# Optimization experiments

Hardware: AMD Instinct MI355X
Metric: run time of the kernel (lower is better)

Reference implementation:

```python
import jax, jax.numpy as jnp
import numpy as np

N_NODES = 100_000
N_EDGES = 1_250_000
IN_FEATS, N_HIDDEN, N_CLASSES = 64, 64, 32


def setup_inputs() -> dict:
    key = jax.random.key(0)
    ks = jax.random.split(key, 8)
    x = jax.random.normal(ks[0], (N_NODES, IN_FEATS), dtype=jnp.float32)
    src = jax.random.randint(ks[1], (N_EDGES,), 0, N_NODES, dtype=jnp.int64)
    dst = jax.random.randint(ks[2], (N_EDGES,), 0, N_NODES, dtype=jnp.int64)
    s1 = 1.0 / np.sqrt(IN_FEATS)
    s2 = 1.0 / np.sqrt(N_HIDDEN)
    W_self1 = jax.random.normal(ks[3], (IN_FEATS, N_HIDDEN), dtype=jnp.float32) * s1
    W_neigh1 = jax.random.normal(ks[4], (IN_FEATS, N_HIDDEN), dtype=jnp.float32) * s1
    b1 = jnp.zeros((N_HIDDEN,), dtype=jnp.float32)
    W_self2 = jax.random.normal(ks[5], (N_HIDDEN, N_CLASSES), dtype=jnp.float32) * s2
    W_neigh2 = jax.random.normal(ks[6], (N_HIDDEN, N_CLASSES), dtype=jnp.float32) * s2
    b2 = jnp.zeros((N_CLASSES,), dtype=jnp.float32)
    return dict(x=x, src=src, dst=dst, W_self1=W_self1, W_neigh1=W_neigh1, b1=b1,
                W_self2=W_self2, W_neigh2=W_neigh2, b2=b2)


def _sage_conv(h, src, dst, W_self, W_neigh, b):
    # mean aggregation over in-neighbors: gather src feats, segment-sum by dst
    n = h.shape[0]
    msg = h[src]  # [E, d] -- dominant memory traffic
    agg = jax.ops.segment_sum(msg, dst, num_segments=n)
    deg = jax.ops.segment_sum(jnp.ones_like(dst, dtype=h.dtype), dst, num_segments=n)
    h_neigh = agg / jnp.maximum(deg, 1.0)[:, None]  # zero-degree nodes get 0 (DGL behavior)
    return h @ W_self + h_neigh @ W_neigh + b


def reference(x, src, dst, W_self1, W_neigh1, b1, W_self2, W_neigh2, b2):
    h = _sage_conv(x, src, dst, W_self1, W_neigh1, b1)
    h = jax.nn.relu(h)
    # dropout(p=0.5) is identity in eval mode
    return _sage_conv(h, src, dst, W_self2, W_neigh2, b2)
```

## Files before the change

### kernel.cpp

```cpp
#include <hip/hip_runtime.h>
#include <hip/hip_bf16.h>


#define NF 64
#define BW 256
#define BSH 8
#define MAXB 512
#define CAPMAX 8192
#define P1_CHUNK 2048
#define H1S 68

typedef __attribute__((ext_vector_type(8))) short short8;
typedef __attribute__((ext_vector_type(8))) unsigned short ushort8v;
typedef __attribute__((ext_vector_type(4))) float floatx4;

__device__ __forceinline__ short bf16hi(float v) {
    __hip_bfloat16 h = __float2bfloat16(v);
    return *(short*)&h;
}
__device__ __forceinline__ float bf2f(short s) {
    __hip_bfloat16 h = *(__hip_bfloat16*)&s;
    return __bfloat162float(h);
}
__device__ __forceinline__ float bits2f(unsigned short u) {
    unsigned int x = ((unsigned int)u) << 16;
    union { unsigned int i; float f; } c; c.i = x; return c.f;
}


__global__ __launch_bounds__(256) void prep_kernel(
        int* __restrict__ gcursor,
        const float* __restrict__ Ws1, const float* __restrict__ Wn1,
        const float* __restrict__ Ws2, const float* __restrict__ Wn2,
        unsigned short* __restrict__ w1p, unsigned short* __restrict__ w2p) {
    const int tid = threadIdx.x;
    if (blockIdx.x == 0) {
        for (int i = tid; i < MAXB; i += 256) gcursor[i] = 0;
        return;
    }
    const int part = blockIdx.x - 1;
    for (int i = tid; i < 32 * 64; i += 256) {
        int n = part * 32 + (i >> 6), k = i & 63;
        float v = (n < 64) ? Ws1[k * 64 + n] : Wn1[k * 64 + (n - 64)];
        short hv = bf16hi(v);
        w1p[n * 64 + k] = (unsigned short)hv;
        w1p[8192 + n * 64 + k] = (unsigned short)bf16hi(v - bf2f(hv));
    }
    for (int i = tid; i < 16 * 64; i += 256) {
        int n = part * 16 + (i >> 6), k = i & 63;
        float v = (n < 32) ? Ws2[k * 32 + n] : Wn2[k * 32 + (n - 32)];
        short hv = bf16hi(v);
        w2p[n * 64 + k] = (unsigned short)hv;
        w2p[4096 + n * 64 + k] = (unsigned short)bf16hi(v - bf2f(hv));
    }
}


__global__ __launch_bounds__(256) void p1_dense1_kernel(
        const int* __restrict__ src, const int* __restrict__ dst,
        int* __restrict__ gcursor, unsigned* __restrict__ bucket,
        int E, int nbuckets, int dblocks,
        const float* __restrict__ X,
        const unsigned short* __restrict__ w1p,
        const float* __restrict__ bias,
        float* __restrict__ outA,
        unsigned short* __restrict__ outB,
        int N) {
    __shared__ int smem_i[2 * MAXB];
    const int tid = threadIdx.x;

    if ((int)blockIdx.x >= dblocks) {
        int* cnt   = smem_i;
        int* cbase = smem_i + MAXB;
        const int bid = blockIdx.x - dblocks;
        const int beg = bid * P1_CHUNK;
        const int end = min(E, beg + P1_CHUNK);
        for (int i = tid; i < nbuckets; i += 256) cnt[i] = 0;
        __syncthreads();
        for (int e = beg + tid; e < end; e += 256)
            atomicAdd(&cnt[dst[e] >> BSH], 1);
        __syncthreads();
        for (int i = tid; i < nbuckets; i += 256) {
            int c = cnt[i];
            cbase[i] = c ? atomicAdd(&gcursor[i], c) : 0;
            cnt[i] = 0;
        }
        __syncthreads();
        for (int e = beg + tid; e < end; e += 256) {
            int d = dst[e];
            int r = d >> BSH;
            int p = cbase[r] + atomicAdd(&cnt[r], 1);
            if (p < CAPMAX)
                bucket[(size_t)r * CAPMAX + p] = ((unsigned)src[e] << BSH) | (unsigned)(d & (BW - 1));
        }
        return;
    }

    constexpr int NT = 8, NSELF = 4;
    const int lane = tid & 63;
    const int wid  = tid >> 6;
    const int m = lane & 15, quad = lane >> 4;
    const int rowblk = blockIdx.x * 128 + wid * 32;

    floatx4 acc[2][NT];
    #pragma unroll
    for (int rt = 0; rt < 2; ++rt)
        #pragma unroll
        for (int t = 0; t < NT; ++t) acc[rt][t] = (floatx4)(0.f);

    short8 ah[2][2], al[2][2];
    #pragma unroll
    for (int rt = 0; rt < 2; ++rt) {
        int r = rowblk + rt * 16 + m;
        if (r >= N) r = N - 1;
        const float* xp = X + (size_t)r * 64 + quad * 8;
        #pragma unroll
        for (int h = 0; h < 2; ++h) {
            floatx4 f0 = *(const floatx4*)(xp + h * 32);
            floatx4 f1 = *(const floatx4*)(xp + h * 32 + 4);
            short8 hi, lo;
            #pragma unroll
            for (int j = 0; j < 4; ++j) {
                short hv = bf16hi(f0[j]);
                hi[j] = hv; lo[j] = bf16hi(f0[j] - bf2f(hv));
                short hv2 = bf16hi(f1[j]);
                hi[4 + j] = hv2; lo[4 + j] = bf16hi(f1[j] - bf2f(hv2));
            }
            ah[rt][h] = hi; al[rt][h] = lo;
        }
    }

    #pragma unroll
    for (int t = 0; t < NT; ++t) {
        int n = t * 16 + m;
        const unsigned short* ph = w1p + n * 64 + quad * 8;
        const unsigned short* pl = ph + 8192;
        #pragma unroll
        for (int h = 0; h < 2; ++h) {
            short8 bh = *(const short8*)(ph + h * 32);
            short8 bl = *(const short8*)(pl + h * 32);
            #pragma unroll
            for (int rt = 0; rt < 2; ++rt) {
                acc[rt][t] = __builtin_amdgcn_mfma_f32_16x16x32_bf16(ah[rt][h], bh, acc[rt][t], 0, 0, 0);
                acc[rt][t] = __builtin_amdgcn_mfma_f32_16x16x32_bf16(al[rt][h], bh, acc[rt][t], 0, 0, 0);
                acc[rt][t] = __builtin_amdgcn_mfma_f32_16x16x32_bf16(ah[rt][h], bl, acc[rt][t], 0, 0, 0);
            }
        }
    }

    #pragma unroll
    for (int rt = 0; rt < 2; ++rt) {
        #pragma unroll
        for (int t = 0; t < NT; ++t) {
            #pragma unroll
            for (int r4 = 0; r4 < 4; ++r4) {
                int row = rowblk + rt * 16 + quad * 4 + r4;
                if (row < N) {
                    if (t < NSELF) {
                        int col = t * 16 + m;
                        outA[(size_t)row * 64 + col] = acc[rt][t][r4] + bias[col];
                    } else {
                        int col = (t - NSELF) * 16 + m;
                        outB[(size_t)row * 64 + col] = (unsigned short)bf16hi(acc[rt][t][r4]);
                    }
                }
            }
        }
    }
}


__global__ __launch_bounds__(256) void p2_csr_kernel(const unsigned* __restrict__ bucket,
                                                     const int* __restrict__ gcursor,
                                                     int* __restrict__ row_start,
                                                     int* __restrict__ csr_src,
                                                     int N, int nbuckets) {
    __shared__ unsigned stage[CAPMAX];
    __shared__ int cnt[BW];
    __shared__ int excl[BW];
    const int r = blockIdx.x;
    const int tid = threadIdx.x;

    int partial = 0;
    for (int i = tid; i < r; i += 256) partial += min(gcursor[i], CAPMAX);
    excl[tid] = partial;
    __syncthreads();
    for (int off = 128; off > 0; off >>= 1) {
        if (tid < off) excl[tid] += excl[tid + off];
        __syncthreads();
    }
    const int base = excl[0];
    const int sz = min(gcursor[r], CAPMAX);
    const unsigned* bsrc = bucket + (size_t)r * CAPMAX;
    __syncthreads();

    cnt[tid] = 0;
    __syncthreads();
    for (int i = tid; i < sz; i += 256) {
        unsigned v = bsrc[i];
        stage[i] = v;
        atomicAdd(&cnt[v & (BW - 1)], 1);
    }
    __syncthreads();
    excl[tid] = cnt[tid];
    __syncthreads();
    for (int off = 1; off < BW; off <<= 1) {
        int v0 = (tid >= off) ? excl[tid - off] : 0;
        __syncthreads();
        excl[tid] += v0;
        __syncthreads();
    }
    int node = r * BW + tid;
    if (node < N) row_start[node] = base + excl[tid] - cnt[tid];
    if (r == nbuckets - 1 && tid == 0) row_start[N] = base + sz;
    __syncthreads();
    cnt[tid] = excl[tid] - cnt[tid];
    __syncthreads();
    for (int i = tid; i < sz; i += 256) {
        unsigned v = stage[i];
        int p = atomicAdd(&cnt[v & (BW - 1)], 1);
        csr_src[base + p] = (int)(v >> BSH);
    }
}


__global__ __launch_bounds__(256) void agg64_d2_kernel(
        const unsigned short* __restrict__ t1n,
        const float* __restrict__ xs,
        const int* __restrict__ row_start,
        const int* __restrict__ csr_src,
        const unsigned short* __restrict__ w2p,
        const float* __restrict__ b2,
        float* __restrict__ outD,
        unsigned short* __restrict__ t2n,
        int N, int E) {
    __shared__ float h1s[16][H1S];
    const int tid = threadIdx.x;
    const int lane = tid & 63;
    const int wid  = tid >> 6;
    const int half = lane >> 5;
    const int g = (lane >> 3) & 3;
    const int c = lane & 7;
    const int nbase = blockIdx.x * 16;

    const int ln0 = wid * 4 + half;
    const int ln1 = ln0 + 2;
    const int n0 = nbase + ln0, n1 = nbase + ln1;
    int beg0 = 0, end0 = 0, beg1 = 0, end1 = 0;
    if (n0 < N) { beg0 = row_start[n0]; end0 = row_start[n0 + 1]; }
    if (n1 < N) { beg1 = row_start[n1]; end1 = row_start[n1 + 1]; }

    float a0[8] = {0.f, 0.f, 0.f, 0.f, 0.f, 0.f, 0.f, 0.f};
    float a1[8] = {0.f, 0.f, 0.f, 0.f, 0.f, 0.f, 0.f, 0.f};
    int j0 = beg0 + g, j1 = beg1 + g;
    const int Em1 = E - 1;
    int i0 = csr_src[min(j0, Em1)];
    int i1 = csr_src[min(j0 + 4, Em1)];
    int i2 = csr_src[min(j1, Em1)];
    int i3 = csr_src[min(j1 + 4, Em1)];
    while ((j0 < end0) || (j1 < end1)) {
        int s0 = ((unsigned)i0 < (unsigned)N) ? i0 : 0;
        int s1 = ((unsigned)i1 < (unsigned)N) ? i1 : 0;
        int s2 = ((unsigned)i2 < (unsigned)N) ? i2 : 0;
        int s3 = ((unsigned)i3 < (unsigned)N) ? i3 : 0;
        ushort8v u0 = *(const ushort8v*)(t1n + (size_t)s0 * 64 + c * 8);
        ushort8v u1 = *(const ushort8v*)(t1n + (size_t)s1 * 64 + c * 8);
        ushort8v u2 = *(const ushort8v*)(t1n + (size_t)s2 * 64 + c * 8);
        ushort8v u3 = *(const ushort8v*)(t1n + (size_t)s3 * 64 + c * 8);
        i0 = csr_src[min(j0 + 8, Em1)];
        i1 = csr_src[min(j0 + 12, Em1)];
        i2 = csr_src[min(j1 + 8, Em1)];
        i3 = csr_src[min(j1 + 12, Em1)];
        const bool c00 = j0 < end0, c01 = j0 + 4 < end0;
        const bool c10 = j1 < end1, c11 = j1 + 4 < end1;
        #pragma unroll
        for (int i = 0; i < 8; ++i) {
            a0[i] += (c00 ? bits2f(u0[i]) : 0.f) + (c01 ? bits2f(u1[i]) : 0.f);
            a1[i] += (c10 ? bits2f(u2[i]) : 0.f) + (c11 ? bits2f(u3[i]) : 0.f);
        }
        j0 += 8; j1 += 8;
    }

    const int m = lane & 15, quad = lane >> 4;
    const int coln = wid * 16 + m;
    const unsigned short* pb = w2p + coln * 64 + quad * 8;
    short8 bhf0 = *(const short8*)(pb);
    short8 bhf1 = *(const short8*)(pb + 32);
    short8 blf0 = *(const short8*)(pb + 4096);
    short8 blf1 = *(const short8*)(pb + 4096 + 32);

    floatx4 x00 = (floatx4)(0.f), x01 = (floatx4)(0.f);
    floatx4 x10 = (floatx4)(0.f), x11 = (floatx4)(0.f);
    if (g == 0) {
        if (n0 < N) {
            const float* p = xs + (size_t)n0 * 64 + c * 8;
            x00 = *(const floatx4*)p; x01 = *(const floatx4*)(p + 4);
        }
        if (n1 < N) {
            const float* p = xs + (size_t)n1 * 64 + c * 8;
            x10 = *(const floatx4*)p; x11 = *(const floatx4*)(p + 4);
        }
    }

    #pragma unroll
    for (int i = 0; i < 8; ++i) {
        float v = a0[i];
        v += __shfl_xor(v, 8);
        v += __shfl_xor(v, 16);
        a0[i] = v;
        float w = a1[i];
        w += __shfl_xor(w, 8);
        w += __shfl_xor(w, 16);
        a1[i] = w;
    }
    if (g == 0) {
        floatx4 h0, h1v;
        if (n0 < N) {
            float invd = 1.0f / fmaxf((float)(end0 - beg0), 1.0f);
            #pragma unroll
            for (int i = 0; i < 4; ++i) {
                h0[i]  = fmaxf(x00[i] + a0[i] * invd, 0.f);
                h1v[i] = fmaxf(x01[i] + a0[4 + i] * invd, 0.f);
            }
        } else { h0 = (floatx4)(0.f); h1v = (floatx4)(0.f); }
        *(floatx4*)&h1s[ln0][c * 8]     = h0;
        *(floatx4*)&h1s[ln0][c * 8 + 4] = h1v;
        if (n1 < N) {
            float invd = 1.0f / fmaxf((float)(end1 - beg1), 1.0f);
            #pragma unroll
            for (int i = 0; i < 4; ++i) {
                h0[i]  = fmaxf(x10[i] + a1[i] * invd, 0.f);
                h1v[i] = fmaxf(x11[i] + a1[4 + i] * invd, 0.f);
            }
        } else { h0 = (floatx4)(0.f); h1v = (floatx4)(0.f); }
        *(floatx4*)&h1s[ln1][c * 8]     = h0;
        *(floatx4*)&h1s[ln1][c * 8 + 4] = h1v;
    }
    __syncthreads();

    short8 ah[2], al[2];
    #pragma unroll
    for (int h = 0; h < 2; ++h) {
        const float* hp = &h1s[m][quad * 8 + h * 32];
        floatx4 f0 = *(const floatx4*)hp;
        floatx4 f1 = *(const floatx4*)(hp + 4);
        short8 hi, lo;
        #pragma unroll
        for (int j = 0; j < 4; ++j) {
            short hv = bf16hi(f0[j]);
            hi[j] = hv; lo[j] = bf16hi(f0[j] - bf2f(hv));
            short hv2 = bf16hi(f1[j]);
            hi[4 + j] = hv2; lo[4 + j] = bf16hi(f1[j] - bf2f(hv2));
        }
        ah[h] = hi; al[h] = lo;
    }
    floatx4 acc2 = (floatx4)(0.f);
    acc2 = __builtin_amdgcn_mfma_f32_16x16x32_bf16(ah[0], bhf0, acc2, 0, 0, 0);
    acc2 = __builtin_amdgcn_mfma_f32_16x16x32_bf16(al[0], bhf0, acc2, 0, 0, 0);
    acc2 = __builtin_amdgcn_mfma_f32_16x16x32_bf16(ah[0], blf0, acc2, 0, 0, 0);
    acc2 = __builtin_amdgcn_mfma_f32_16x16x32_bf16(ah[1], bhf1, acc2, 0, 0, 0);
    acc2 = __builtin_amdgcn_mfma_f32_16x16x32_bf16(al[1], bhf1, acc2, 0, 0, 0);
    acc2 = __builtin_amdgcn_mfma_f32_16x16x32_bf16(ah[1], blf1, acc2, 0, 0, 0);
    #pragma unroll
    for (int r4 = 0; r4 < 4; ++r4) {
        int node = nbase + quad * 4 + r4;
        if (node < N) {
            if (coln < 32) outD[(size_t)node * 32 + coln] = acc2[r4] + b2[coln];
            else t2n[(size_t)node * 32 + (coln - 32)] = (unsigned short)bf16hi(acc2[r4]);
        }
    }
}


__global__ __launch_bounds__(256) void agg32_kernel(float* io,
                                                    const unsigned short* __restrict__ t2n,
                                                    const int* __restrict__ row_start,
                                                    const int* __restrict__ csr_src,
                                                    int N, int E) {
    const int tid = threadIdx.x;
    const int lane = tid & 63;
    const int wid = tid >> 6;
    const int slot = lane >> 4;
    const int g = (lane >> 2) & 3;
    const int c = lane & 3;
    const int n = blockIdx.x * 16 + wid * 4 + slot;

    int beg = 0, end = 0;
    if (n < N) { beg = row_start[n]; end = row_start[n + 1]; }

    floatx4 s0v = (floatx4)(0.f), s1v = (floatx4)(0.f);
    size_t o = (size_t)n * 32 + c * 8;
    if (n < N && g == 0) {
        s0v = *(const floatx4*)(io + o);
        s1v = *(const floatx4*)(io + o + 4);
    }

    float acc[8] = {0.f, 0.f, 0.f, 0.f, 0.f, 0.f, 0.f, 0.f};
    const int Em1 = E - 1;
    for (int j = beg + g; j < end; j += 8) {
        int j2 = j + 4;
        int s0 = csr_src[j];
        int s1 = csr_src[min(j2, Em1)];
        s0 = ((unsigned)s0 < (unsigned)N) ? s0 : 0;
        s1 = ((unsigned)s1 < (unsigned)N) ? s1 : 0;
        ushort8v u0 = *(const ushort8v*)(t2n + (size_t)s0 * 32 + c * 8);
        ushort8v u1 = *(const ushort8v*)(t2n + (size_t)s1 * 32 + c * 8);
        const bool c1 = j2 < end;
        #pragma unroll
        for (int i = 0; i < 8; ++i)
            acc[i] += bits2f(u0[i]) + (c1 ? bits2f(u1[i]) : 0.f);
    }
    #pragma unroll
    for (int i = 0; i < 8; ++i) {
        float v = acc[i];
        v += __shfl_xor(v, 4);
        v += __shfl_xor(v, 8);
        acc[i] = v;
    }
    if (n < N && g == 0) {
        float inv = 1.0f / fmaxf((float)(end - beg), 1.0f);
        floatx4 r0, r1;
        #pragma unroll
        for (int i = 0; i < 4; ++i) {
            r0[i] = s0v[i] + acc[i] * inv;
            r1[i] = s1v[i] + acc[4 + i] * inv;
        }
        *(floatx4*)(io + o) = r0;
        *(floatx4*)(io + o + 4) = r1;
    }
}


__global__ __launch_bounds__(256) void deg_kernel(const int* __restrict__ dst,
                                                  float* __restrict__ deg, int E) {
    int e = blockIdx.x * blockDim.x + threadIdx.x;
    if (e < E) atomicAdd(&deg[dst[e]], 1.0f);
}

__global__ __launch_bounds__(256) void agg_atomic_kernel(const float* __restrict__ feats,
                                                         const int* __restrict__ src,
                                                         const int* __restrict__ dst,
                                                         float* __restrict__ agg, int E) {
    int tid = blockIdx.x * blockDim.x + threadIdx.x;
    if (tid >= E * NF) return;
    int e = tid >> 6, f = tid & 63;
    atomicAdd(&agg[(size_t)dst[e] * NF + f], feats[(size_t)src[e] * NF + f]);
}

__global__ __launch_bounds__(256) void layer1_fb_kernel(const float* __restrict__ x,
                                                        const float* __restrict__ agg,
                                                        const float* __restrict__ deg,
                                                        const float* __restrict__ Wself,
                                                        const float* __restrict__ Wneigh,
                                                        const float* __restrict__ b,
                                                        float* __restrict__ h1, int N) {
    int tid = blockIdx.x * blockDim.x + threadIdx.x;
    if (tid >= N * NF) return;
    int n = tid >> 6, c = tid & 63;
    float inv = 1.0f / fmaxf(deg[n], 1.0f);
    const float* xrow = x + (size_t)n * NF;
    const float* arow = agg + (size_t)n * NF;
    float acc = b[c];
    #pragma unroll
    for (int k = 0; k < NF; ++k) {
        acc += xrow[k] * Wself[k * NF + c];
        acc += (arow[k] * inv) * Wneigh[k * NF + c];
    }
    h1[tid] = fmaxf(acc, 0.f);
}

__global__ __launch_bounds__(256) void layer2_fb_kernel(const float* __restrict__ h1,
                                                        const float* __restrict__ agg,
                                                        const float* __restrict__ deg,
                                                        const float* __restrict__ Wself,
                                                        const float* __restrict__ Wneigh,
                                                        const float* __restrict__ b,
                                                        float* __restrict__ out, int N) {
    int tid = blockIdx.x * blockDim.x + threadIdx.x;
    if (tid >= N * 32) return;
    int n = tid >> 5, c = tid & 31;
    float inv = 1.0f / fmaxf(deg[n], 1.0f);
    const float* hrow = h1 + (size_t)n * NF;
    const float* arow = agg + (size_t)n * NF;
    float acc = b[c];
    #pragma unroll
    for (int k = 0; k < NF; ++k) {
        acc += hrow[k] * Wself[k * 32 + c];
        acc += (arow[k] * inv) * Wneigh[k * 32 + c];
    }
    out[tid] = acc;
}


extern "C" void kernel_launch(void* const* d_in, const int* in_sizes, int n_in,
                              void* d_out, int out_size, void* d_ws, size_t ws_size,
                              hipStream_t stream) {
    const float* x        = (const float*)d_in[0];
    const int*   src      = (const int*)d_in[1];
    const int*   dst      = (const int*)d_in[2];
    const float* W_self1  = (const float*)d_in[3];
    const float* W_neigh1 = (const float*)d_in[4];
    const float* b1       = (const float*)d_in[5];
    const float* W_self2  = (const float*)d_in[6];
    const float* W_neigh2 = (const float*)d_in[7];
    const float* b2       = (const float*)d_in[8];
    float* out = (float*)d_out;

    const int N = in_sizes[0] / NF;
    const int E = in_sizes[1];
    const int nbuckets = (N + BW - 1) / BW;

    const size_t rsPad = ((size_t)N + 8) & ~7ull;
    int* gcursor   = (int*)d_ws;
    unsigned short* w2p = (unsigned short*)(gcursor + MAXB);
    unsigned short* w1p = w2p + 8192;
    int* row_start = (int*)(w1p + 16384);
    int* csr_src   = row_start + rsPad;
    uintptr_t pa = (uintptr_t)(csr_src + (((size_t)E + 7) & ~7ull));
    pa = (pa + 127) & ~(uintptr_t)127;
    float* bufA = (float*)pa;
    unsigned* bucket = (unsigned*)bufA;
    unsigned short* t1n = (unsigned short*)(bufA + (size_t)N * NF);
    unsigned short* t2n = t1n + (size_t)N * NF;
    size_t need = (size_t)((char*)(t2n + (size_t)N * 32) - (char*)d_ws);

    bool fast = ws_size >= need
             && E > 0
             && nbuckets <= MAXB
             && (size_t)nbuckets * CAPMAX <= (size_t)N * NF
             && (size_t)E * 2 / (size_t)nbuckets <= CAPMAX
             && N < (1 << 24)
             && out_size >= N * 32;

    if (fast) {
        prep_kernel<<<5, 256, 0, stream>>>(gcursor, W_self1, W_neigh1,
                                           W_self2, W_neigh2, w1p, w2p);
        int dblocks  = (N + 127) / 128;
        int p1blocks = (E + P1_CHUNK - 1) / P1_CHUNK;
        unsigned* bucket2 = (unsigned*)(t2n + (((size_t)N * 32 + 63) & ~63ull));
        size_t need2 = (size_t)((char*)(bucket2 + (size_t)nbuckets * CAPMAX) - (char*)d_ws);
        if (ws_size >= need2) {
            p1_dense1_kernel<<<dblocks + p1blocks, 256, 0, stream>>>(
                src, dst, gcursor, bucket2, E, nbuckets, dblocks,
                x, w1p, b1, bufA, t1n, N);
            p2_csr_kernel<<<nbuckets, 256, 0, stream>>>(bucket2, gcursor,
                                                        row_start, csr_src, N, nbuckets);
        } else {
            p1_dense1_kernel<<<p1blocks, 256, 0, stream>>>(
                src, dst, gcursor, bucket, E, nbuckets, 0,
                x, w1p, b1, bufA, t1n, N);
            p2_csr_kernel<<<nbuckets, 256, 0, stream>>>(bucket, gcursor,
                                                        row_start, csr_src, N, nbuckets);
            p1_dense1_kernel<<<dblocks, 256, 0, stream>>>(
                src, dst, gcursor, bucket, E, nbuckets, dblocks,
                x, w1p, b1, bufA, t1n, N);
        }
        agg64_d2_kernel<<<(N + 15) / 16, 256, 0, stream>>>(
            t1n, bufA, row_start, csr_src, w2p, b2, out, t2n, N, E);
        agg32_kernel<<<(N + 15) / 16, 256, 0, stream>>>(out, t2n,
                                                        row_start, csr_src, N, E);
    } else {
        float* deg = (float*)d_ws;
        float* agg = deg + N;
        float* h1  = agg + (size_t)N * NF;
        hipMemsetAsync(deg, 0, (size_t)(N + (size_t)N * NF) * sizeof(float), stream);
        deg_kernel<<<(E + 255) / 256, 256, 0, stream>>>(dst, deg, E);
        int at = E * NF;
        agg_atomic_kernel<<<(at + 255) / 256, 256, 0, stream>>>(x, src, dst, agg, E);
        layer1_fb_kernel<<<(N * NF + 255) / 256, 256, 0, stream>>>(x, agg, deg, W_self1,
                                                                   W_neigh1, b1, h1, N);
        hipMemsetAsync(agg, 0, (size_t)N * NF * sizeof(float), stream);
        agg_atomic_kernel<<<(at + 255) / 256, 256, 0, stream>>>(h1, src, dst, agg, E);
        layer2_fb_kernel<<<(N * 32 + 255) / 256, 256, 0, stream>>>(h1, agg, deg, W_self2,
                                                                   W_neigh2, b2, out, N);
    }
}
```

Measured before the change: 203.6 us.

## Fuse all stages into one persistent cooperative kernel with grid syncs

Replaces the five separate kernel launches (prep, bucket+dense1, CSR build, agg64+dense2, agg32) with a single cooperative persistent kernel that loops over virtual blocks and uses grid.sync between phases, falling back to the old launches if cooperative launch fails. The aim is to remove launch gaps and tail idle time between kernels. The CSR build also drops its 32KB shared staging buffer and re-reads buckets from global memory, which shrinks shared memory so more blocks fit per CU. The trade-off is grid-wide barrier overhead, a grid size limited by occupancy of the fused kernel's register use, and extra global reads in the CSR phase.

```diff
diff --git a/kernel.cpp b/kernel.cpp
--- a/kernel.cpp
+++ b/kernel.cpp
@@ -1,6 +1,9 @@
 #include <hip/hip_runtime.h>
 #include <hip/hip_bf16.h>
-
+#include <hip/hip_cooperative_groups.h>
+
+
+namespace cg = cooperative_groups;
 
 #define NF 64
 #define BW 256
@@ -28,79 +31,73 @@
 }
 
 
-__global__ __launch_bounds__(256) void prep_kernel(
-        int* __restrict__ gcursor,
+__device__ __forceinline__ void prep_body(int v, int* __restrict__ gcursor,
         const float* __restrict__ Ws1, const float* __restrict__ Wn1,
         const float* __restrict__ Ws2, const float* __restrict__ Wn2,
         unsigned short* __restrict__ w1p, unsigned short* __restrict__ w2p) {
     const int tid = threadIdx.x;
-    if (blockIdx.x == 0) {
+    if (v == 0) {
         for (int i = tid; i < MAXB; i += 256) gcursor[i] = 0;
         return;
     }
-    const int part = blockIdx.x - 1;
+    const int part = v - 1;
     for (int i = tid; i < 32 * 64; i += 256) {
         int n = part * 32 + (i >> 6), k = i & 63;
-        float v = (n < 64) ? Ws1[k * 64 + n] : Wn1[k * 64 + (n - 64)];
-        short hv = bf16hi(v);
+        float w = (n < 64) ? Ws1[k * 64 + n] : Wn1[k * 64 + (n - 64)];
+        short hv = bf16hi(w);
         w1p[n * 64 + k] = (unsigned short)hv;
-        w1p[8192 + n * 64 + k] = (unsigned short)bf16hi(v - bf2f(hv));
+        w1p[8192 + n * 64 + k] = (unsigned short)bf16hi(w - bf2f(hv));
     }
     for (int i = tid; i < 16 * 64; i += 256) {
         int n = part * 16 + (i >> 6), k = i & 63;
-        float v = (n < 32) ? Ws2[k * 32 + n] : Wn2[k * 32 + (n - 32)];
-        short hv = bf16hi(v);
+        float w = (n < 32) ? Ws2[k * 32 + n] : Wn2[k * 32 + (n - 32)];
+        short hv = bf16hi(w);
         w2p[n * 64 + k] = (unsigned short)hv;
-        w2p[4096 + n * 64 + k] = (unsigned short)bf16hi(v - bf2f(hv));
-    }
-}
-
-
-__global__ __launch_bounds__(256) void p1_dense1_kernel(
+        w2p[4096 + n * 64 + k] = (unsigned short)bf16hi(w - bf2f(hv));
+    }
+}
+
+__device__ __forceinline__ void p1_body(int bid, int* __restrict__ pool,
         const int* __restrict__ src, const int* __restrict__ dst,
         int* __restrict__ gcursor, unsigned* __restrict__ bucket,
-        int E, int nbuckets, int dblocks,
-        const float* __restrict__ X,
-        const unsigned short* __restrict__ w1p,
+        int E, int nbuckets) {
+    int* cnt   = pool;
+    int* cbase = pool + MAXB;
+    const int tid = threadIdx.x;
+    __syncthreads();
+    const int beg = bid * P1_CHUNK;
+    const int end = min(E, beg + P1_CHUNK);
+    for (int i = tid; i < nbuckets; i += 256) cnt[i] = 0;
+    __syncthreads();
+    for (int e = beg + tid; e < end; e += 256)
+        atomicAdd(&cnt[dst[e] >> BSH], 1);
+    __syncthreads();
+    for (int i = tid; i < nbuckets; i += 256) {
+        int c = cnt[i];
+        cbase[i] = c ? atomicAdd(&gcursor[i], c) : 0;
+        cnt[i] = 0;
+    }
+    __syncthreads();
+    for (int e = beg + tid; e < end; e += 256) {
+        int d = dst[e];
+        int r = d >> BSH;
+        int p = cbase[r] + atomicAdd(&cnt[r], 1);
+        if (p < CAPMAX)
+            bucket[(size_t)r * CAPMAX + p] = ((unsigned)src[e] << BSH) | (unsigned)(d & (BW - 1));
+    }
+    __syncthreads();
+}
+
+__device__ __forceinline__ void dense1_body(int vb,
+        const float* __restrict__ X, const unsigned short* __restrict__ w1p,
         const float* __restrict__ bias,
-        float* __restrict__ outA,
-        unsigned short* __restrict__ outB,
-        int N) {
-    __shared__ int smem_i[2 * MAXB];
+        float* __restrict__ outA, unsigned short* __restrict__ outB, int N) {
+    constexpr int NT = 8, NSELF = 4;
     const int tid = threadIdx.x;
-
-    if ((int)blockIdx.x >= dblocks) {
-        int* cnt   = smem_i;
-        int* cbase = smem_i + MAXB;
-        const int bid = blockIdx.x - dblocks;
-        const int beg = bid * P1_CHUNK;
-        const int end = min(E, beg + P1_CHUNK);
-        for (int i = tid; i < nbuckets; i += 256) cnt[i] = 0;
-        __syncthreads();
-        for (int e = beg + tid; e < end; e += 256)
-            atomicAdd(&cnt[dst[e] >> BSH], 1);
-        __syncthreads();
-        for (int i = tid; i < nbuckets; i += 256) {
-            int c = cnt[i];
-            cbase[i] = c ? atomicAdd(&gcursor[i], c) : 0;
-            cnt[i] = 0;
-        }
-        __syncthreads();
-        for (int e = beg + tid; e < end; e += 256) {
-            int d = dst[e];
-            int r = d >> BSH;
-            int p = cbase[r] + atomicAdd(&cnt[r], 1);
-            if (p < CAPMAX)
-                bucket[(size_t)r * CAPMAX + p] = ((unsigned)src[e] << BSH) | (unsigned)(d & (BW - 1));
-        }
-        return;
-    }
-
-    constexpr int NT = 8, NSELF = 4;
     const int lane = tid & 63;
     const int wid  = tid >> 6;
     const int m = lane & 15, quad = lane >> 4;
-    const int rowblk = blockIdx.x * 128 + wid * 32;
+    const int rowblk = vb * 128 + wid * 32;
 
     floatx4 acc[2][NT];
     #pragma unroll
@@ -169,17 +166,14 @@
     }
 }
 
-
-__global__ __launch_bounds__(256) void p2_csr_kernel(const unsigned* __restrict__ bucket,
-                                                     const int* __restrict__ gcursor,
-                                                     int* __restrict__ row_start,
-                                                     int* __restrict__ csr_src,
-                                                     int N, int nbuckets) {
-    __shared__ unsigned stage[CAPMAX];
-    __shared__ int cnt[BW];
-    __shared__ int excl[BW];
-    const int r = blockIdx.x;
+__device__ __forceinline__ void p2_body(int r, int* __restrict__ pool,
+        const unsigned* __restrict__ bucket, const int* __restrict__ gcursor,
+        int* __restrict__ row_start, int* __restrict__ csr_src,
+        int N, int nbuckets) {
+    int* cnt  = pool;
+    int* excl = pool + BW;
     const int tid = threadIdx.x;
+    __syncthreads();
 
     int partial = 0;
     for (int i = tid; i < r; i += 256) partial += min(gcursor[i], CAPMAX);
@@ -196,11 +190,8 @@
 
     cnt[tid] = 0;
     __syncthreads();
-    for (int i = tid; i < sz; i += 256) {
-        unsigned v = bsrc[i];
-        stage[i] = v;
-        atomicAdd(&cnt[v & (BW - 1)], 1);
-    }
+    for (int i = tid; i < sz; i += 256)
+        atomicAdd(&cnt[bsrc[i] & (BW - 1)], 1);
     __syncthreads();
     excl[tid] = cnt[tid];
     __syncthreads();
@@ -217,31 +208,27 @@
     cnt[tid] = excl[tid] - cnt[tid];
     __syncthreads();
     for (int i = tid; i < sz; i += 256) {
-        unsigned v = stage[i];
+        unsigned v = bsrc[i];
         int p = atomicAdd(&cnt[v & (BW - 1)], 1);
         csr_src[base + p] = (int)(v >> BSH);
     }
-}
-
-
-__global__ __launch_bounds__(256) void agg64_d2_kernel(
-        const unsigned short* __restrict__ t1n,
-        const float* __restrict__ xs,
-        const int* __restrict__ row_start,
-        const int* __restrict__ csr_src,
-        const unsigned short* __restrict__ w2p,
+    __syncthreads();
+}
+
+__device__ __forceinline__ void agg64_body(int vb, float (*__restrict__ h1s)[H1S],
+        const unsigned short* __restrict__ t1n, const float* __restrict__ xs,
+        const int* __restrict__ row_start, const int* __restrict__ csr_src,
         const float* __restrict__ b2,
-        float* __restrict__ outD,
-        unsigned short* __restrict__ t2n,
-        int N, int E) {
-    __shared__ float h1s[16][H1S];
+        float* __restrict__ outD, unsigned short* __restrict__ t2n,
+        int N, int E,
+        short8 bhf0, short8 bhf1, short8 blf0, short8 blf1) {
     const int tid = threadIdx.x;
     const int lane = tid & 63;
     const int wid  = tid >> 6;
     const int half = lane >> 5;
     const int g = (lane >> 3) & 3;
     const int c = lane & 7;
-    const int nbase = blockIdx.x * 16;
+    const int nbase = vb * 16;
 
     const int ln0 = wid * 4 + half;
     const int ln1 = ln0 + 2;
@@ -283,11 +270,6 @@
 
     const int m = lane & 15, quad = lane >> 4;
     const int coln = wid * 16 + m;
-    const unsigned short* pb = w2p + coln * 64 + quad * 8;
-    short8 bhf0 = *(const short8*)(pb);
-    short8 bhf1 = *(const short8*)(pb + 32);
-    short8 blf0 = *(const short8*)(pb + 4096);
-    short8 blf1 = *(const short8*)(pb + 4096 + 32);
 
     floatx4 x00 = (floatx4)(0.f), x01 = (floatx4)(0.f);
     floatx4 x10 = (floatx4)(0.f), x11 = (floatx4)(0.f);
@@ -369,21 +351,19 @@
             else t2n[(size_t)node * 32 + (coln - 32)] = (unsigned short)bf16hi(acc2[r4]);
         }
     }
-}
-
-
-__global__ __launch_bounds__(256) void agg32_kernel(float* io,
-                                                    const unsigned short* __restrict__ t2n,
-                                                    const int* __restrict__ row_start,
-                                                    const int* __restrict__ csr_src,
-                                                    int N, int E) {
+    __syncthreads();
+}
+
+__device__ __forceinline__ void agg32_body(int vb, float* __restrict__ io,
+        const unsigned short* __restrict__ t2n, const int* __restrict__ row_start,
+        const int* __restrict__ csr_src, int N, int E) {
     const int tid = threadIdx.x;
     const int lane = tid & 63;
     const int wid = tid >> 6;
     const int slot = lane >> 4;
     const int g = (lane >> 2) & 3;
     const int c = lane & 3;
-    const int n = blockIdx.x * 16 + wid * 4 + slot;
+    const int n = vb * 16 + wid * 4 + slot;
 
     int beg = 0, end = 0;
     if (n < N) { beg = row_start[n]; end = row_start[n + 1]; }
@@ -431,6 +411,131 @@
 }
 
 
+__global__ __launch_bounds__(256) void fused_kernel(
+        const int* __restrict__ src, const int* __restrict__ dst,
+        int* __restrict__ gcursor, unsigned* __restrict__ bucket,
+        const float* __restrict__ X,
+        const float* __restrict__ Ws1, const float* __restrict__ Wn1,
+        const float* __restrict__ b1,
+        const float* __restrict__ Ws2, const float* __restrict__ Wn2,
+        const float* __restrict__ b2,
+        unsigned short* __restrict__ w1p, unsigned short* __restrict__ w2p,
+        float* __restrict__ bufA, unsigned short* __restrict__ t1n,
+        int* __restrict__ row_start, int* __restrict__ csr_src,
+        float* __restrict__ outD, unsigned short* __restrict__ t2n,
+        int N, int E, int nbuckets, int dblocks, int p1blocks) {
+    __shared__ __align__(16) int pool[1088];
+    cg::grid_group grid = cg::this_grid();
+    const int gb = gridDim.x;
+    const int bid = blockIdx.x;
+
+    for (int v = bid; v < 5; v += gb)
+        prep_body(v, gcursor, Ws1, Wn1, Ws2, Wn2, w1p, w2p);
+    __threadfence();
+    grid.sync();
+
+    const int ph1 = dblocks + p1blocks;
+    for (int v = bid; v < ph1; v += gb) {
+        if (v < dblocks) dense1_body(v, X, w1p, b1, bufA, t1n, N);
+        else p1_body(v - dblocks, pool, src, dst, gcursor, bucket, E, nbuckets);
+    }
+    __threadfence();
+    grid.sync();
+
+    for (int v = bid; v < nbuckets; v += gb)
+        p2_body(v, pool, bucket, gcursor, row_start, csr_src, N, nbuckets);
+    __threadfence();
+    grid.sync();
+
+    {
+        const int lane = threadIdx.x & 63;
+        const int wid = threadIdx.x >> 6;
+        const int m = lane & 15, quad = lane >> 4;
+        const int coln = wid * 16 + m;
+        const unsigned short* pb = w2p + coln * 64 + quad * 8;
+        short8 bhf0 = *(const short8*)(pb);
+        short8 bhf1 = *(const short8*)(pb + 32);
+        short8 blf0 = *(const short8*)(pb + 4096);
+        short8 blf1 = *(const short8*)(pb + 4096 + 32);
+        const int ntiles = (N + 15) / 16;
+        float (*h1s)[H1S] = (float (*)[H1S])pool;
+        for (int v = bid; v < ntiles; v += gb)
+            agg64_body(v, h1s, t1n, bufA, row_start, csr_src, b2, outD, t2n,
+                       N, E, bhf0, bhf1, blf0, blf1);
+    }
+    __threadfence();
+    grid.sync();
+
+    {
+        const int ntiles = (N + 15) / 16;
+        for (int v = bid; v < ntiles; v += gb)
+            agg32_body(v, outD, t2n, row_start, csr_src, N, E);
+    }
+}
+
+
+__global__ __launch_bounds__(256) void prep_kernel(
+        int* __restrict__ gcursor,
+        const float* __restrict__ Ws1, const float* __restrict__ Wn1,
+        const float* __restrict__ Ws2, const float* __restrict__ Wn2,
+        unsigned short* __restrict__ w1p, unsigned short* __restrict__ w2p) {
+    prep_body(blockIdx.x, gcursor, Ws1, Wn1, Ws2, Wn2, w1p, w2p);
+}
+
+__global__ __launch_bounds__(256) void p1_dense1_kernel(
+        const int* __restrict__ src, const int* __restrict__ dst,
+        int* __restrict__ gcursor, unsigned* __restrict__ bucket,
+        int E, int nbuckets, int dblocks,
+        const float* __restrict__ X,
+        const unsigned short* __restrict__ w1p,
+        const float* __restrict__ bias,
+        float* __restrict__ outA, unsigned short* __restrict__ outB,
+        int N) {
+    __shared__ __align__(16) int pool[2 * MAXB];
+    if ((int)blockIdx.x >= dblocks)
+        p1_body(blockIdx.x - dblocks, pool, src, dst, gcursor, bucket, E, nbuckets);
+    else
+        dense1_body(blockIdx.x, X, w1p, bias, outA, outB, N);
+}
+
+__global__ __launch_bounds__(256) void p2_csr_kernel(const unsigned* __restrict__ bucket,
+                                                     const int* __restrict__ gcursor,
+                                                     int* __restrict__ row_start,
+                                                     int* __restrict__ csr_src,
+                                                     int N, int nbuckets) {
+    __shared__ __align__(16) int pool[2 * BW];
+    p2_body(blockIdx.x, pool, bucket, gcursor, row_start, csr_src, N, nbuckets);
+}
+
+__global__ __launch_bounds__(256) void agg64_d2_kernel(
+        const unsigned short* __restrict__ t1n, const float* __restrict__ xs,
+        const int* __restrict__ row_start, const int* __restrict__ csr_src,
+        const unsigned short* __restrict__ w2p, const float* __restrict__ b2,
+        float* __restrict__ outD, unsigned short* __restrict__ t2n,
+        int N, int E) {
+    __shared__ __align__(16) float h1s[16][H1S];
+    const int lane = threadIdx.x & 63;
+    const int wid = threadIdx.x >> 6;
+    const int m = lane & 15, quad = lane >> 4;
+    const int coln = wid * 16 + m;
+    const unsigned short* pb = w2p + coln * 64 + quad * 8;
+    short8 bhf0 = *(const short8*)(pb);
+    short8 bhf1 = *(const short8*)(pb + 32);
+    short8 blf0 = *(const short8*)(pb + 4096);
+    short8 blf1 = *(const short8*)(pb + 4096 + 32);
+    agg64_body(blockIdx.x, h1s, t1n, xs, row_start, csr_src, b2, outD, t2n,
+               N, E, bhf0, bhf1, blf0, blf1);
+}
+
+__global__ __launch_bounds__(256) void agg32_kernel(float* io,
+                                                    const unsigned short* __restrict__ t2n,
+                                                    const int* __restrict__ row_start,
+                                                    const int* __restrict__ csr_src,
+                                                    int N, int E) {
+    agg32_body(blockIdx.x, io, t2n, row_start, csr_src, N, E);
+}
+
+
 __global__ __launch_bounds__(256) void deg_kernel(const int* __restrict__ dst,
                                                   float* __restrict__ deg, int E) {
     int e = blockIdx.x * blockDim.x + threadIdx.x;
@@ -533,32 +638,77 @@
              && out_size >= N * 32;
 
     if (fast) {
-        prep_kernel<<<5, 256, 0, stream>>>(gcursor, W_self1, W_neigh1,
-                                           W_self2, W_neigh2, w1p, w2p);
         int dblocks  = (N + 127) / 128;
         int p1blocks = (E + P1_CHUNK - 1) / P1_CHUNK;
         unsigned* bucket2 = (unsigned*)(t2n + (((size_t)N * 32 + 63) & ~63ull));
         size_t need2 = (size_t)((char*)(bucket2 + (size_t)nbuckets * CAPMAX) - (char*)d_ws);
-        if (ws_size >= need2) {
-            p1_dense1_kernel<<<dblocks + p1blocks, 256, 0, stream>>>(
-                src, dst, gcursor, bucket2, E, nbuckets, dblocks,
-                x, w1p, b1, bufA, t1n, N);
-            p2_csr_kernel<<<nbuckets, 256, 0, stream>>>(bucket2, gcursor,
-                                                        row_start, csr_src, N, nbuckets);
-        } else {
-            p1_dense1_kernel<<<p1blocks, 256, 0, stream>>>(
-                src, dst, gcursor, bucket, E, nbuckets, 0,
-                x, w1p, b1, bufA, t1n, N);
-            p2_csr_kernel<<<nbuckets, 256, 0, stream>>>(bucket, gcursor,
-                                                        row_start, csr_src, N, nbuckets);
-            p1_dense1_kernel<<<dblocks, 256, 0, stream>>>(
-                src, dst, gcursor, bucket, E, nbuckets, dblocks,
-                x, w1p, b1, bufA, t1n, N);
-        }
-        agg64_d2_kernel<<<(N + 15) / 16, 256, 0, stream>>>(
-            t1n, bufA, row_start, csr_src, w2p, b2, out, t2n, N, E);
-        agg32_kernel<<<(N + 15) / 16, 256, 0, stream>>>(out, t2n,
-                                                        row_start, csr_src, N, E);
+        const bool disjoint = ws_size >= need2;
+
+        static int s_grid = -2;
+        if (s_grid == -2) {
+            int dev = 0; hipGetDevice(&dev);
+            int coop = 0;
+            hipDeviceGetAttribute(&coop, hipDeviceAttributeCooperativeLaunch, dev);
+            if (coop) {
+                int cus = 0, bpc = 0;
+                hipDeviceGetAttribute(&cus, hipDeviceAttributeMultiprocessorCount, dev);
+                hipOccupancyMaxActiveBlocksPerMultiprocessor(&bpc, fused_kernel, 256, 0);
+                s_grid = (cus > 0 && bpc > 0) ? cus * bpc : -1;
+            } else s_grid = -1;
+        }
+
+        bool launched = false;
+        if (disjoint && s_grid >= 64) {
+            const int* src_a = src; const int* dst_a = dst;
+            int* gcur_a = gcursor; unsigned* buck_a = bucket2;
+            const float* x_a = x;
+            const float* ws1_a = W_self1; const float* wn1_a = W_neigh1;
+            const float* b1_a = b1;
+            const float* ws2_a = W_self2; const float* wn2_a = W_neigh2;
+            const float* b2_a = b2;
+            unsigned short* w1p_a = w1p; unsigned short* w2p_a = w2p;
+            float* bufA_a = bufA; unsigned short* t1n_a = t1n;
+            int* rs_a = row_start; int* csr_a = csr_src;
+            float* out_a = out; unsigned short* t2n_a = t2n;
+            int N_a = N, E_a = E, nb_a = nbuckets, db_a = dblocks, pb_a = p1blocks;
+            void* kargs[] = {
+                (void*)&src_a, (void*)&dst_a, (void*)&gcur_a, (void*)&buck_a,
+                (void*)&x_a, (void*)&ws1_a, (void*)&wn1_a, (void*)&b1_a,
+                (void*)&ws2_a, (void*)&wn2_a, (void*)&b2_a,
+                (void*)&w1p_a, (void*)&w2p_a, (void*)&bufA_a, (void*)&t1n_a,
+                (void*)&rs_a, (void*)&csr_a, (void*)&out_a, (void*)&t2n_a,
+                (void*)&N_a, (void*)&E_a, (void*)&nb_a, (void*)&db_a, (void*)&pb_a };
+            hipError_t err = hipLaunchCooperativeKernel(fused_kernel,
+                                                        dim3(s_grid), dim3(256),
+                                                        kargs, 0, stream);
+            if (err == hipSuccess) launched = true;
+            else (void)hipGetLastError();
+        }
+
+        if (!launched) {
+            prep_kernel<<<5, 256, 0, stream>>>(gcursor, W_self1, W_neigh1,
+                                               W_self2, W_neigh2, w1p, w2p);
+            if (disjoint) {
+                p1_dense1_kernel<<<dblocks + p1blocks, 256, 0, stream>>>(
+                    src, dst, gcursor, bucket2, E, nbuckets, dblocks,
+                    x, w1p, b1, bufA, t1n, N);
+                p2_csr_kernel<<<nbuckets, 256, 0, stream>>>(bucket2, gcursor,
+                                                            row_start, csr_src, N, nbuckets);
+            } else {
+                p1_dense1_kernel<<<p1blocks, 256, 0, stream>>>(
+                    src, dst, gcursor, bucket, E, nbuckets, 0,
+                    x, w1p, b1, bufA, t1n, N);
+                p2_csr_kernel<<<nbuckets, 256, 0, stream>>>(bucket, gcursor,
+                                                            row_start, csr_src, N, nbuckets);
+                p1_dense1_kernel<<<dblocks, 256, 0, stream>>>(
+                    src, dst, gcursor, bucket, E, nbuckets, dblocks,
+                    x, w1p, b1, bufA, t1n, N);
+            }
+            agg64_d2_kernel<<<(N + 15) / 16, 256, 0, stream>>>(
+                t1n, bufA, row_start, csr_src, w2p, b2, out, t2n, N, E);
+            agg32_kernel<<<(N + 15) / 16, 256, 0, stream>>>(out, t2n,
+                                                            row_start, csr_src, N, E);
+        }
     } else {
         float* deg = (float*)d_ws;
         float* agg = deg + N;
```

Result: slower. 542.4 us (+166.4%).

## Move layer-1 self GEMM into aggregation kernel and fold weight prep into p1

Applied to the files above, without the earlier changes.

Removes the separate prep kernel. Gcursor is now zeroed with a memset, and weight packing runs in extra blocks of the first kernel. The dense kernel now computes only the neighbor projection, with W_neigh1 packed into LDS per block. The layer-1 self projection (X@W_self1+b1) is recomputed by MFMA inside the aggregation kernel, so the fp32 self-term buffer of N×64 floats is no longer written and read back. In exchange, the aggregation kernel rereads X and does extra MFMA work, and each dense block repacks the weights in LDS.

```diff
diff --git a/kernel.cpp b/kernel.cpp
--- a/kernel.cpp
+++ b/kernel.cpp
@@ -9,6 +9,7 @@
 #define CAPMAX 8192
 #define P1_CHUNK 2048
 #define H1S 68
+#define WST 72
 
 typedef __attribute__((ext_vector_type(8))) short short8;
 typedef __attribute__((ext_vector_type(8))) unsigned short ushort8v;
@@ -28,46 +29,41 @@
 }
 
 
-__global__ __launch_bounds__(256) void prep_kernel(
-        int* __restrict__ gcursor,
-        const float* __restrict__ Ws1, const float* __restrict__ Wn1,
-        const float* __restrict__ Ws2, const float* __restrict__ Wn2,
-        unsigned short* __restrict__ w1p, unsigned short* __restrict__ w2p) {
-    const int tid = threadIdx.x;
-    if (blockIdx.x == 0) {
-        for (int i = tid; i < MAXB; i += 256) gcursor[i] = 0;
-        return;
-    }
-    const int part = blockIdx.x - 1;
-    for (int i = tid; i < 32 * 64; i += 256) {
-        int n = part * 32 + (i >> 6), k = i & 63;
-        float v = (n < 64) ? Ws1[k * 64 + n] : Wn1[k * 64 + (n - 64)];
-        short hv = bf16hi(v);
-        w1p[n * 64 + k] = (unsigned short)hv;
-        w1p[8192 + n * 64 + k] = (unsigned short)bf16hi(v - bf2f(hv));
-    }
-    for (int i = tid; i < 16 * 64; i += 256) {
-        int n = part * 16 + (i >> 6), k = i & 63;
-        float v = (n < 32) ? Ws2[k * 32 + n] : Wn2[k * 32 + (n - 32)];
-        short hv = bf16hi(v);
-        w2p[n * 64 + k] = (unsigned short)hv;
-        w2p[4096 + n * 64 + k] = (unsigned short)bf16hi(v - bf2f(hv));
-    }
-}
-
-
-__global__ __launch_bounds__(256) void p1_dense1_kernel(
+__global__ __launch_bounds__(256) void d1p1_kernel(
         const int* __restrict__ src, const int* __restrict__ dst,
         int* __restrict__ gcursor, unsigned* __restrict__ bucket,
         int E, int nbuckets, int dblocks,
         const float* __restrict__ X,
-        const unsigned short* __restrict__ w1p,
-        const float* __restrict__ bias,
-        float* __restrict__ outA,
+        const float* __restrict__ Wn1,
         unsigned short* __restrict__ outB,
-        int N) {
-    __shared__ int smem_i[2 * MAXB];
+        int N,
+        const float* __restrict__ Ws1,
+        const float* __restrict__ Ws2,
+        const float* __restrict__ Wn2,
+        unsigned short* __restrict__ w1p,
+        unsigned short* __restrict__ w2p) {
+    __shared__ __align__(16) int smem_i[4608];
     const int tid = threadIdx.x;
+    const int packBase = dblocks + ((E + P1_CHUNK - 1) / P1_CHUNK);
+
+    if ((int)blockIdx.x >= packBase) {
+        const int part = blockIdx.x - packBase;
+        for (int i = tid; i < 16 * 64; i += 256) {
+            int n = part * 16 + (i >> 6), k = i & 63;
+            float v = Ws1[k * 64 + n];
+            short hv = bf16hi(v);
+            w1p[n * 64 + k] = (unsigned short)hv;
+            w1p[4096 + n * 64 + k] = (unsigned short)bf16hi(v - bf2f(hv));
+        }
+        for (int i = tid; i < 16 * 64; i += 256) {
+            int n = part * 16 + (i >> 6), k = i & 63;
+            float v = (n < 32) ? Ws2[k * 32 + n] : Wn2[k * 32 + (n - 32)];
+            short hv = bf16hi(v);
+            w2p[n * 64 + k] = (unsigned short)hv;
+            w2p[4096 + n * 64 + k] = (unsigned short)bf16hi(v - bf2f(hv));
+        }
+        return;
+    }
 
     if ((int)blockIdx.x >= dblocks) {
         int* cnt   = smem_i;
@@ -96,7 +92,17 @@
         return;
     }
 
-    constexpr int NT = 8, NSELF = 4;
+    constexpr int NT = 4;
+    unsigned short* wh = (unsigned short*)smem_i;
+    unsigned short* wl = wh + 64 * WST;
+    for (int i = tid; i < 64 * 64; i += 256) {
+        int c = i & 63, k = i >> 6;
+        float v = Wn1[k * 64 + c];
+        short hv = bf16hi(v);
+        wh[c * WST + k] = (unsigned short)hv;
+        wl[c * WST + k] = (unsigned short)bf16hi(v - bf2f(hv));
+    }
+
     const int lane = tid & 63;
     const int wid  = tid >> 6;
     const int m = lane & 15, quad = lane >> 4;
@@ -129,12 +135,13 @@
             ah[rt][h] = hi; al[rt][h] = lo;
         }
     }
+    __syncthreads();
 
     #pragma unroll
     for (int t = 0; t < NT; ++t) {
-        int n = t * 16 + m;
-        const unsigned short* ph = w1p + n * 64 + quad * 8;
-        const unsigned short* pl = ph + 8192;
+        int c = t * 16 + m;
+        const unsigned short* ph = wh + c * WST + quad * 8;
+        const unsigned short* pl = wl + c * WST + quad * 8;
         #pragma unroll
         for (int h = 0; h < 2; ++h) {
             short8 bh = *(const short8*)(ph + h * 32);
@@ -156,13 +163,8 @@
             for (int r4 = 0; r4 < 4; ++r4) {
                 int row = rowblk + rt * 16 + quad * 4 + r4;
                 if (row < N) {
-                    if (t < NSELF) {
-                        int col = t * 16 + m;
-                        outA[(size_t)row * 64 + col] = acc[rt][t][r4] + bias[col];
-                    } else {
-                        int col = (t - NSELF) * 16 + m;
-                        outB[(size_t)row * 64 + col] = (unsigned short)bf16hi(acc[rt][t][r4]);
-                    }
+                    int col = t * 16 + m;
+                    outB[(size_t)row * 64 + col] = (unsigned short)bf16hi(acc[rt][t][r4]);
                 }
             }
         }
@@ -224,17 +226,19 @@
 }
 
 
-__global__ __launch_bounds__(256) void agg64_d2_kernel(
+__global__ __launch_bounds__(256) void agg64s_d2_kernel(
         const unsigned short* __restrict__ t1n,
-        const float* __restrict__ xs,
+        const float* __restrict__ X,
         const int* __restrict__ row_start,
         const int* __restrict__ csr_src,
+        const unsigned short* __restrict__ w1p,
         const unsigned short* __restrict__ w2p,
+        const float* __restrict__ b1,
         const float* __restrict__ b2,
         float* __restrict__ outD,
         unsigned short* __restrict__ t2n,
         int N, int E) {
-    __shared__ float h1s[16][H1S];
+    __shared__ __align__(16) float h1s[16][H1S];
     const int tid = threadIdx.x;
     const int lane = tid & 63;
     const int wid  = tid >> 6;
@@ -242,6 +246,14 @@
     const int g = (lane >> 3) & 3;
     const int c = lane & 7;
     const int nbase = blockIdx.x * 16;
+
+    const int m = lane & 15, quad = lane >> 4;
+    const int coln = wid * 16 + m;
+    const unsigned short* pb = w2p + coln * 64 + quad * 8;
+    short8 bhf0 = *(const short8*)(pb);
+    short8 bhf1 = *(const short8*)(pb + 32);
+    short8 blf0 = *(const short8*)(pb + 4096);
+    short8 blf1 = *(const short8*)(pb + 4096 + 32);
 
     const int ln0 = wid * 4 + half;
     const int ln1 = ln0 + 2;
@@ -281,26 +293,30 @@
         j0 += 8; j1 += 8;
     }
 
-    const int m = lane & 15, quad = lane >> 4;
-    const int coln = wid * 16 + m;
-    const unsigned short* pb = w2p + coln * 64 + quad * 8;
-    short8 bhf0 = *(const short8*)(pb);
-    short8 bhf1 = *(const short8*)(pb + 32);
-    short8 blf0 = *(const short8*)(pb + 4096);
-    short8 blf1 = *(const short8*)(pb + 4096 + 32);
-
-    floatx4 x00 = (floatx4)(0.f), x01 = (floatx4)(0.f);
-    floatx4 x10 = (floatx4)(0.f), x11 = (floatx4)(0.f);
-    if (g == 0) {
-        if (n0 < N) {
-            const float* p = xs + (size_t)n0 * 64 + c * 8;
-            x00 = *(const floatx4*)p; x01 = *(const floatx4*)(p + 4);
-        }
-        if (n1 < N) {
-            const float* p = xs + (size_t)n1 * 64 + c * 8;
-            x10 = *(const floatx4*)p; x11 = *(const floatx4*)(p + 4);
-        }
-    }
+    int rA = nbase + m;
+    if (rA >= N) rA = N - 1;
+    const float* xp = X + (size_t)rA * 64 + quad * 8;
+    short8 sah[2], sal[2];
+    #pragma unroll
+    for (int h = 0; h < 2; ++h) {
+        floatx4 f0 = *(const floatx4*)(xp + h * 32);
+        floatx4 f1 = *(const floatx4*)(xp + h * 32 + 4);
+        short8 hi, lo;
+        #pragma unroll
+        for (int j = 0; j < 4; ++j) {
+            short hv = bf16hi(f0[j]);
+            hi[j] = hv; lo[j] = bf16hi(f0[j] - bf2f(hv));
+            short hv2 = bf16hi(f1[j]);
+            hi[4 + j] = hv2; lo[4 + j] = bf16hi(f1[j] - bf2f(hv2));
+        }
+        sah[h] = hi; sal[h] = lo;
+    }
+    const unsigned short* pbs = w1p + coln * 64 + quad * 8;
+    short8 sbh0 = *(const short8*)(pbs);
+    short8 sbh1 = *(const short8*)(pbs + 32);
+    short8 sbl0 = *(const short8*)(pbs + 4096);
+    short8 sbl1 = *(const short8*)(pbs + 4096 + 32);
+    const float bias1 = b1[coln];
 
     #pragma unroll
     for (int i = 0; i < 8; ++i) {
@@ -319,8 +335,8 @@
             float invd = 1.0f / fmaxf((float)(end0 - beg0), 1.0f);
             #pragma unroll
             for (int i = 0; i < 4; ++i) {
-                h0[i]  = fmaxf(x00[i] + a0[i] * invd, 0.f);
-                h1v[i] = fmaxf(x01[i] + a0[4 + i] * invd, 0.f);
+                h0[i]  = a0[i] * invd;
+                h1v[i] = a0[4 + i] * invd;
             }
         } else { h0 = (floatx4)(0.f); h1v = (floatx4)(0.f); }
         *(floatx4*)&h1s[ln0][c * 8]     = h0;
@@ -329,12 +345,27 @@
             float invd = 1.0f / fmaxf((float)(end1 - beg1), 1.0f);
             #pragma unroll
             for (int i = 0; i < 4; ++i) {
-                h0[i]  = fmaxf(x10[i] + a1[i] * invd, 0.f);
-                h1v[i] = fmaxf(x11[i] + a1[4 + i] * invd, 0.f);
+                h0[i]  = a1[i] * invd;
+                h1v[i] = a1[4 + i] * invd;
             }
         } else { h0 = (floatx4)(0.f); h1v = (floatx4)(0.f); }
         *(floatx4*)&h1s[ln1][c * 8]     = h0;
         *(floatx4*)&h1s[ln1][c * 8 + 4] = h1v;
+    }
+    __syncthreads();
+
+    floatx4 accS = (floatx4)(0.f);
+    accS = __builtin_amdgcn_mfma_f32_16x16x32_bf16(sah[0], sbh0, accS, 0, 0, 0);
+    accS = __builtin_amdgcn_mfma_f32_16x16x32_bf16(sal[0], sbh0, accS, 0, 0, 0);
+    accS = __builtin_amdgcn_mfma_f32_16x16x32_bf16(sah[0], sbl0, accS, 0, 0, 0);
+    accS = __builtin_amdgcn_mfma_f32_16x16x32_bf16(sah[1], sbh1, accS, 0, 0, 0);
+    accS = __builtin_amdgcn_mfma_f32_16x16x32_bf16(sal[1], sbh1, accS, 0, 0, 0);
+    accS = __builtin_amdgcn_mfma_f32_16x16x32_bf16(sah[1], sbl1, accS, 0, 0, 0);
+    #pragma unroll
+    for (int r4 = 0; r4 < 4; ++r4) {
+        int row = quad * 4 + r4;
+        float val = (accS[r4] + bias1) + h1s[row][coln];
+        h1s[row][coln] = fmaxf(val, 0.f);
     }
     __syncthreads();
 
@@ -514,49 +545,36 @@
     int* gcursor   = (int*)d_ws;
     unsigned short* w2p = (unsigned short*)(gcursor + MAXB);
     unsigned short* w1p = w2p + 8192;
-    int* row_start = (int*)(w1p + 16384);
+    int* row_start = (int*)(w1p + 8192);
     int* csr_src   = row_start + rsPad;
     uintptr_t pa = (uintptr_t)(csr_src + (((size_t)E + 7) & ~7ull));
     pa = (pa + 127) & ~(uintptr_t)127;
-    float* bufA = (float*)pa;
-    unsigned* bucket = (unsigned*)bufA;
-    unsigned short* t1n = (unsigned short*)(bufA + (size_t)N * NF);
+    unsigned short* t1n = (unsigned short*)pa;
     unsigned short* t2n = t1n + (size_t)N * NF;
-    size_t need = (size_t)((char*)(t2n + (size_t)N * 32) - (char*)d_ws);
+    uintptr_t pb = (uintptr_t)(t2n + (size_t)N * 32);
+    pb = (pb + 63) & ~(uintptr_t)63;
+    unsigned* bucket = (unsigned*)pb;
+    size_t need = (size_t)((char*)(bucket + (size_t)nbuckets * CAPMAX) - (char*)d_ws);
 
     bool fast = ws_size >= need
-             && E > 0
+             && E > 0 && N > 0
              && nbuckets <= MAXB
-             && (size_t)nbuckets * CAPMAX <= (size_t)N * NF
              && (size_t)E * 2 / (size_t)nbuckets <= CAPMAX
              && N < (1 << 24)
              && out_size >= N * 32;
 
     if (fast) {
-        prep_kernel<<<5, 256, 0, stream>>>(gcursor, W_self1, W_neigh1,
-                                           W_self2, W_neigh2, w1p, w2p);
-        int dblocks  = (N + 127) / 128;
-        int p1blocks = (E + P1_CHUNK - 1) / P1_CHUNK;
-        unsigned* bucket2 = (unsigned*)(t2n + (((size_t)N * 32 + 63) & ~63ull));
-        size_t need2 = (size_t)((char*)(bucket2 + (size_t)nbuckets * CAPMAX) - (char*)d_ws);
-        if (ws_size >= need2) {
-            p1_dense1_kernel<<<dblocks + p1blocks, 256, 0, stream>>>(
-                src, dst, gcursor, bucket2, E, nbuckets, dblocks,
-                x, w1p, b1, bufA, t1n, N);
-            p2_csr_kernel<<<nbuckets, 256, 0, stream>>>(bucket2, gcursor,
-                                                        row_start, csr_src, N, nbuckets);
-        } else {
-            p1_dense1_kernel<<<p1blocks, 256, 0, stream>>>(
-                src, dst, gcursor, bucket, E, nbuckets, 0,
-                x, w1p, b1, bufA, t1n, N);
-            p2_csr_kernel<<<nbuckets, 256, 0, stream>>>(bucket, gcursor,
-                                                        row_start, csr_src, N, nbuckets);
-            p1_dense1_kernel<<<dblocks, 256, 0, stream>>>(
-                src, dst, gcursor, bucket, E, nbuckets, dblocks,
-                x, w1p, b1, bufA, t1n, N);
-        }
-        agg64_d2_kernel<<<(N + 15) / 16, 256, 0, stream>>>(
-            t1n, bufA, row_start, csr_src, w2p, b2, out, t2n, N, E);
+        const int dblocks  = (N + 127) / 128;
+        const int p1blocks = (E + P1_CHUNK - 1) / P1_CHUNK;
+        hipMemsetAsync(gcursor, 0, MAXB * sizeof(int), stream);
+        d1p1_kernel<<<dblocks + p1blocks + 4, 256, 0, stream>>>(
+            src, dst, gcursor, bucket, E, nbuckets, dblocks,
+            x, W_neigh1, t1n, N,
+            W_self1, W_self2, W_neigh2, w1p, w2p);
+        p2_csr_kernel<<<nbuckets, 256, 0, stream>>>(bucket, gcursor,
+                                                    row_start, csr_src, N, nbuckets);
+        agg64s_d2_kernel<<<(N + 15) / 16, 256, 0, stream>>>(
+            t1n, x, row_start, csr_src, w1p, w2p, b1, b2, out, t2n, N, E);
         agg32_kernel<<<(N + 15) / 16, 256, 0, stream>>>(out, t2n,
                                                         row_start, csr_src, N, E);
     } else {
```

Measured after the change: 204.0 us. Within noise of the previous version (+0.2%).
